# Kernel tuning notes

Hardware: AMD Instinct MI355X
Metric: run time of the kernel (lower is better)

Reference implementation:

```python
import jax, jax.numpy as jnp
import numpy as np

B, V, C = 2, 6, 96
D, H, W = 48, 48, 48
TH, TW = 96, 96
EPS = 1e-5


def _trilinear_sample_zeros(vol, gx, gy, gz):
    # vol: [B,C,D,H,W]; gx/gy/gz: normalized coords [D,H,W]; align_corners=False, zeros padding
    Dd, Hh, Ww = vol.shape[2], vol.shape[3], vol.shape[4]
    ix = ((gx + 1.0) * Ww - 1.0) * 0.5
    iy = ((gy + 1.0) * Hh - 1.0) * 0.5
    iz = ((gz + 1.0) * Dd - 1.0) * 0.5
    x0 = jnp.floor(ix); y0 = jnp.floor(iy); z0 = jnp.floor(iz)
    tx, ty, tz = ix - x0, iy - y0, iz - z0
    out = jnp.zeros(vol.shape, vol.dtype)
    for dz in (0, 1):
        for dy in (0, 1):
            for dx in (0, 1):
                xc, yc, zc = x0 + dx, y0 + dy, z0 + dz
                w = ((tx if dx else 1.0 - tx) * (ty if dy else 1.0 - ty)
                     * (tz if dz else 1.0 - tz))
                inb = ((xc >= 0) & (xc < Ww) & (yc >= 0) & (yc < Hh)
                       & (zc >= 0) & (zc < Dd))
                xi = jnp.clip(xc, 0, Ww - 1).astype(jnp.int32)
                yi = jnp.clip(yc, 0, Hh - 1).astype(jnp.int32)
                zi = jnp.clip(zc, 0, Dd - 1).astype(jnp.int32)
                val = vol[:, :, zi, yi, xi]  # [B,C,D,H,W]
                out = out + val * (w * inb)[None, None]
    return out


def _resize_bilinear(img, oh, ow):
    # torch F.interpolate(mode='bilinear', align_corners=False) semantics
    h, w = img.shape[-2], img.shape[-1]
    def idx(n_in, n_out):
        scale = n_in / n_out
        src = jnp.maximum(scale * (jnp.arange(n_out) + 0.5) - 0.5, 0.0)
        i0 = jnp.clip(jnp.floor(src).astype(jnp.int32), 0, n_in - 1)
        i1 = jnp.clip(i0 + 1, 0, n_in - 1)
        return i0, i1, (src - i0).astype(img.dtype)
    y0, y1, ty = idx(h, oh)
    x0, x1, tx = idx(w, ow)
    rows = img[..., y0, :] * (1.0 - ty)[:, None] + img[..., y1, :] * ty[:, None]
    return rows[..., x0] * (1.0 - tx) + rows[..., x1] * tx


def _project_one_view(vol, theta):
    # base grid per torch affine_grid(align_corners=False): pixel-center coords in [-1,1]
    zc = (jnp.arange(D) + 0.5) * (2.0 / D) - 1.0
    yc = (jnp.arange(H) + 0.5) * (2.0 / H) - 1.0
    xc = (jnp.arange(W) + 0.5) * (2.0 / W) - 1.0
    Z, Y, X = jnp.meshgrid(zc, yc, xc, indexing='ij')  # [D,H,W]
    c, s = jnp.cos(theta), jnp.sin(theta)
    gx = c * X + s * Z   # rotation about Y axis, rows [c,0,s],[0,1,0],[-s,0,c]
    gy = Y
    gz = -s * X + c * Z
    rotated = _trilinear_sample_zeros(vol, gx, gy, gz)  # [B,C,D,H,W]
    feat2d = rotated.mean(axis=2)                       # depth mean -> [B,C,H,W]
    return _resize_bilinear(feat2d, TH, TW)             # [B,C,TH,TW]


def _post(x, conv1_w, bn_gamma, bn_beta, conv2_w, conv2_b):
    dn = ('NCHW', 'OIHW', 'NCHW')
    x = jax.lax.conv_general_dilated(x, conv1_w, (1, 1), 'SAME', dimension_numbers=dn)
    mu = x.mean(axis=(0, 2, 3), keepdims=True)
    var = ((x - mu) ** 2).mean(axis=(0, 2, 3), keepdims=True)  # biased var, train-mode BN
    x = (x - mu) * jax.lax.rsqrt(var + EPS)
    x = x * bn_gamma[None, :, None, None] + bn_beta[None, :, None, None]
    x = jax.nn.gelu(x, approximate=False)
    x = jax.lax.conv_general_dilated(x, conv2_w, (1, 1), 'SAME', dimension_numbers=dn)
    return x + conv2_b[None, :, None, None]


def setup_inputs() -> dict:
    key = jax.random.key(0)
    k0, k1, k2 = jax.random.split(key, 3)
    voxel_tokens = jax.random.normal(k0, (B, D * H * W, C), jnp.float32)
    view_angles = jnp.linspace(0.0, 2.0 * np.pi, V + 1)[:-1].astype(jnp.float32)
    conv1_w = jax.random.normal(k1, (C, C, 3, 3), jnp.float32) / np.sqrt(C * 9.0)
    bn_gamma = jnp.ones((C,), jnp.float32)
    bn_beta = jnp.zeros((C,), jnp.float32)
    conv2_w = jax.random.normal(k2, (C, C, 1, 1), jnp.float32) / np.sqrt(C)
    conv2_b = jnp.zeros((C,), jnp.float32)
    return dict(voxel_tokens=voxel_tokens, view_angles=view_angles,
                conv1_w=conv1_w, bn_gamma=bn_gamma, bn_beta=bn_beta,
                conv2_w=conv2_w, conv2_b=conv2_b)


def reference(voxel_tokens, view_angles, conv1_w, bn_gamma, bn_beta, conv2_w, conv2_b):
    b = voxel_tokens.shape[0]
    vol = voxel_tokens.transpose(0, 2, 1).reshape(b, C, D, H, W)
    feats = jax.vmap(lambda th: _project_one_view(vol, th))(view_angles)  # [V,B,C,TH,TW]
    # BN stats are computed per-view (torch applies self.post inside the view loop)
    posted = jax.vmap(lambda f: _post(f, conv1_w, bn_gamma, bn_beta, conv2_w, conv2_b))(feats)
    return posted.transpose(1, 0, 2, 3, 4)  # [B,V,C,TH,TW]
```

## Files before the change

### kernel.cpp

```cpp
#include <hip/hip_runtime.h>
#include <math.h>

#define Bn 2
#define Vn 6
#define Cn 96
#define Dn 48
#define Hn 48
#define Wn 48
#define THn 96
#define TWn 96
#define EPSf 1e-5f

#define PD 98
#define NCI8 12

typedef __attribute__((ext_vector_type(8))) short s8v;
typedef __attribute__((ext_vector_type(4))) float f4v;

__device__ __forceinline__ unsigned short f2bf(float f) {
    unsigned int u = __builtin_bit_cast(unsigned int, f);
    u += 0x7FFFu + ((u >> 16) & 1u);
    return (unsigned short)(u >> 16);
}
__device__ __forceinline__ float bf2f(unsigned short h) {
    unsigned int u = ((unsigned int)h) << 16;
    return __builtin_bit_cast(float, u);
}
__device__ __forceinline__ void unpack8(uint4 r, float* f) {
    unsigned int w[4] = {r.x, r.y, r.z, r.w};
#pragma unroll
    for (int j = 0; j < 8; ++j)
        f[j] = bf2f((unsigned short)((w[j >> 1] >> ((j & 1) * 16)) & 0xFFFFu));
}
__device__ __forceinline__ uint4 pack8(const unsigned short* o) {
    uint4 pk;
    pk.x = (unsigned int)o[0] | ((unsigned int)o[1] << 16);
    pk.y = (unsigned int)o[2] | ((unsigned int)o[3] << 16);
    pk.z = (unsigned int)o[4] | ((unsigned int)o[5] << 16);
    pk.w = (unsigned int)o[6] | ((unsigned int)o[7] << 16);
    return pk;
}

__device__ __forceinline__ float gelu_f(float y) {
    float z = y * 0.70710678118654752f;
    float a = fabsf(z);
    float t = __builtin_amdgcn_rcpf(fmaf(0.3275911f, a, 1.0f));
    float e = __builtin_amdgcn_exp2f(-1.4426950408889634f * a * a);
    float p = t * fmaf(t, fmaf(t, fmaf(t, fmaf(t, 1.061405429f,
                                               -1.453152027f),
                                       1.421413741f),
                               -0.284496736f),
                       0.254829592f);
    float er = fmaf(-p, e, 1.0f);
    er = copysignf(er, z);
    return 0.5f * y * (1.0f + er);
}

__global__ __launch_bounds__(256) void k_pre(const float* __restrict__ tokens,
                                             unsigned short* __restrict__ tokB,
                                             const float* __restrict__ w1,
                                             const float* __restrict__ w2,
                                             unsigned short* __restrict__ wAtP,
                                             unsigned short* __restrict__ wCP,
                                             const float* __restrict__ angles,
                                             float4* __restrict__ wtabW,
                                             int4* __restrict__ wtabO) {
    if (blockIdx.x < 10368) {
        int idx = blockIdx.x * 256 + threadIdx.x;
        size_t base = (size_t)idx * 8;
        float4 f0 = *(const float4*)(tokens + base);
        float4 f1 = *(const float4*)(tokens + base + 4);
        unsigned short o[8] = {f2bf(f0.x), f2bf(f0.y), f2bf(f0.z), f2bf(f0.w),
                               f2bf(f1.x), f2bf(f1.y), f2bf(f1.z), f2bf(f1.w)};
        *(uint4*)(&tokB[base]) = pack8(o);
    } else if (blockIdx.x < 10728) {
        int i = (blockIdx.x - 10368) * 256 + threadIdx.x;
        if (i < 82944) {
            int e = i & 7;
            int u = i >> 3;
            int co = u % 96;
            int u2 = u / 96;
            int ci8 = u2 % NCI8;
            int tap = u2 / NCI8;
            wAtP[i] = f2bf(w1[(co * 96 + ci8 * 8 + e) * 9 + tap]);
        } else if (i < 92160) {
            int j = i - 82944;
            int e = j & 7;
            int u = j >> 3;
            int co = u % 96;
            int ci8 = u / 96;
            wCP[j] = f2bf(w2[co * 96 + ci8 * 8 + e]);
        }
    } else {
        int e = (blockIdx.x - 10728) * 256 + threadIdx.x;
        if (e >= 13824) return;
        int z = e % 48;
        int r = e / 48;
        int x = r % 48;
        int v = r / 48;

        float th = angles[v];
        float ct = cosf(th), st = sinf(th);
        float xr = (float)x + 0.5f - 24.0f;
        float zr = (float)z + 0.5f - 24.0f;
        float ix = ct * xr + st * zr + 23.5f;
        float iz = -st * xr + ct * zr + 23.5f;

        float x0f = floorf(ix), z0f = floorf(iz);
        float tx = ix - x0f, tz = iz - z0f;
        int x0 = (int)x0f, z0 = (int)z0f;
        float wx[2] = {1.0f - tx, tx};
        float wz[2] = {1.0f - tz, tz};

        float w[4];
        int o[4];
#pragma unroll
        for (int dz = 0; dz < 2; ++dz) {
            int zc = z0 + dz;
            bool zin = (zc >= 0) && (zc < Dn);
            int zi = min(max(zc, 0), Dn - 1);
#pragma unroll
            for (int dx = 0; dx < 2; ++dx) {
                int xc = x0 + dx;
                bool xin = (xc >= 0) && (xc < Wn);
                int xi = min(max(xc, 0), Wn - 1);
                int k = dz * 2 + dx;
                w[k] = wx[dx] * wz[dz] * ((zin && xin) ? 1.0f : 0.0f) * (1.0f / 48.0f);
                o[k] = (zi * 221184 + xi * 96) * 2;
            }
        }
        wtabW[e] = (float4){w[0], w[1], w[2], w[3]};
        wtabO[e] = (int4){o[0], o[1], o[2], o[3]};
    }
}

__global__ __launch_bounds__(256) void k_feat6(const unsigned short* __restrict__ tokB,
                                               const float4* __restrict__ wtabW,
                                               const int4* __restrict__ wtabO,
                                               unsigned short* __restrict__ featP) {
    int gid = blockIdx.x;
    int xcd = gid & 7;
    int pos = gid >> 3;
    int vblk = xcd * 648 + pos;
    int group = vblk / 9;
    int inner = vblk - group * 9;
    int v = group % 6;
    int by = group / 6;
    int y = by % 48;
    int b = by / 48;
    int vb = v * 2 + b;

    int t = threadIdx.x;
    int l = t & 63;
    int h = l >> 4;
    int s0 = inner * 64 + (t >> 6) * 16 + (l & 15);
    int c8 = s0 % NCI8;
    int x = s0 / NCI8;

    int tb0 = (v * 48 + x) * 48 + h * 12;
    const float4* tw = wtabW + tb0;
    const int4* to = wtabO + tb0;
    const char* tb = (const char*)tokB +
                     ((size_t)b * 10616832 + (size_t)y * 4608 + c8 * 8) * 2;

    float af[8] = {0.f, 0.f, 0.f, 0.f, 0.f, 0.f, 0.f, 0.f};
#pragma unroll 4
    for (int k = 0; k < 12; ++k) {
        float4 w = tw[k];
        int4 o = to[k];
        uint4 r0 = *(const uint4*)(tb + o.x);
        uint4 r1 = *(const uint4*)(tb + o.y);
        uint4 r2 = *(const uint4*)(tb + o.z);
        uint4 r3 = *(const uint4*)(tb + o.w);
        float f0[8], f1[8], f2[8], f3[8];
        unpack8(r0, f0); unpack8(r1, f1); unpack8(r2, f2); unpack8(r3, f3);
#pragma unroll
        for (int j = 0; j < 8; ++j) {
            af[j] += w.x * f0[j] + w.y * f1[j];
            af[j] += w.z * f2[j] + w.w * f3[j];
        }
    }
#pragma unroll
    for (int j = 0; j < 8; ++j) {
        af[j] += __shfl_xor(af[j], 16);
        af[j] += __shfl_xor(af[j], 32);
    }

    if (h == 0) {
        unsigned short o[8];
#pragma unroll
        for (int j = 0; j < 8; ++j) o[j] = f2bf(af[j]);
        size_t off = (((size_t)vb * Hn + y) * NCI8 + c8) * Wn + x;
        *(uint4*)(&featP[off * 8]) = pack8(o);
    }
}

__global__ __launch_bounds__(256) void k_resize(const unsigned short* __restrict__ featP,
                                                unsigned short* __restrict__ rz) {
    if (blockIdx.x >= 5184) {
        int hid = (blockIdx.x - 5184) * 256 + threadIdx.x;
        if (hid >= 55872) return;
        int p = hid % 388;
        int r2 = hid / 388;
        int c8 = r2 % NCI8;
        int vb = r2 / NCI8;
        int py, px;
        if (p < 98)      { py = 0;  px = p; }
        else if (p < 196){ py = 97; px = p - 98; }
        else { int q = p - 196; py = 1 + (q >> 1); px = (q & 1) ? 97 : 0; }
        size_t off = (((size_t)vb * PD + py) * NCI8 + c8) * PD + px;
        *(uint4*)(&rz[off * 8]) = (uint4){0u, 0u, 0u, 0u};
        return;
    }
    int idx = blockIdx.x * 256 + threadIdx.x;
    int x = idx % TWn;
    int r = idx / TWn;
    int c8i = r % NCI8; r /= NCI8;
    int y = r % THn;
    int vb = r / THn;

    float sy = fmaxf(0.5f * (y + 0.5f) - 0.5f, 0.0f);
    int y0 = min((int)sy, Hn - 1);
    int y1 = min(y0 + 1, Hn - 1);
    float ty = sy - (float)y0;
    float sx = fmaxf(0.5f * (x + 0.5f) - 0.5f, 0.0f);
    int x0 = min((int)sx, Wn - 1);
    int x1 = min(x0 + 1, Wn - 1);
    float tx = sx - (float)x0;

    const unsigned short* fb = featP + ((size_t)vb * Hn * NCI8 + c8i) * Wn * 8;
    const unsigned short* r0 = fb + (size_t)y0 * (NCI8 * Wn * 8);
    const unsigned short* r1 = fb + (size_t)y1 * (NCI8 * Wn * 8);
    uint4 q00 = *(const uint4*)(r0 + (size_t)x0 * 8);
    uint4 q01 = *(const uint4*)(r0 + (size_t)x1 * 8);
    uint4 q10 = *(const uint4*)(r1 + (size_t)x0 * 8);
    uint4 q11 = *(const uint4*)(r1 + (size_t)x1 * 8);
    float f00[8], f01[8], f10[8], f11[8];
    unpack8(q00, f00); unpack8(q01, f01); unpack8(q10, f10); unpack8(q11, f11);

    float w00 = (1.f - ty) * (1.f - tx), w01 = (1.f - ty) * tx;
    float w10 = ty * (1.f - tx),         w11 = ty * tx;

    unsigned short o[8];
#pragma unroll
    for (int j = 0; j < 8; ++j)
        o[j] = f2bf(w00 * f00[j] + w01 * f01[j] + w10 * f10[j] + w11 * f11[j]);

    size_t off = (((size_t)vb * PD + (y + 1)) * NCI8 + c8i) * PD + (x + 1);
    *(uint4*)(&rz[off * 8]) = pack8(o);
}

__global__ __launch_bounds__(256) void k_conv1(const unsigned short* __restrict__ rz,
                                               const unsigned short* __restrict__ wAtP,
                                               unsigned short* __restrict__ co1) {
    int blk = blockIdx.x;
    int n0 = blk * 64;
    int vb = n0 / 9216;
    int nl0 = n0 - vb * 9216;

    int t = threadIdx.x;
    int wv = t >> 6;
    int ch = wv & 1;
    int ns = wv >> 1;
    int l = t & 63;
    int l15 = l & 15, q = l >> 4;

    int nt0 = nl0 + ns * 32;
    int nl[2];
    const unsigned short* pB[2];
#pragma unroll
    for (int i = 0; i < 2; ++i) {
        nl[i] = nt0 + i * 16 + l15;
        int y = nl[i] / 96, x = nl[i] - y * 96;
        pB[i] = rz + ((((size_t)vb * PD + y) * NCI8) * PD + x) * 8;
    }

    f4v acc[2][3];
#pragma unroll
    for (int i = 0; i < 2; ++i)
#pragma unroll
        for (int mt = 0; mt < 3; ++mt) acc[i][mt] = (f4v){0.f, 0.f, 0.f, 0.f};

#pragma unroll
    for (int ks = 0; ks < 3; ++ks) {
        int ci8 = ks * 4 + q;
        const unsigned short* pb0 = pB[0] + (size_t)ci8 * (PD * 8);
        const unsigned short* pb1 = pB[1] + (size_t)ci8 * (PD * 8);
        const unsigned short* pa = wAtP + ((size_t)ci8 * 96 + ch * 48 + l15) * 8;
#pragma unroll
        for (int tap = 0; tap < 9; ++tap) {
            int dy = tap / 3, dx = tap % 3;
            size_t toff = ((size_t)dy * (NCI8 * PD) + dx) * 8;
            s8v b0 = *(const s8v*)(pb0 + toff);
            s8v b1 = *(const s8v*)(pb1 + toff);
            const unsigned short* ap = pa + (size_t)tap * (NCI8 * 96 * 8);
#pragma unroll
            for (int mt = 0; mt < 3; ++mt) {
                s8v a = *(const s8v*)(ap + (size_t)mt * (16 * 8));
                acc[0][mt] = __builtin_amdgcn_mfma_f32_16x16x32_bf16(a, b0, acc[0][mt], 0, 0, 0);
                acc[1][mt] = __builtin_amdgcn_mfma_f32_16x16x32_bf16(a, b1, acc[1][mt], 0, 0, 0);
            }
        }
    }

#pragma unroll
    for (int i = 0; i < 2; ++i) {
#pragma unroll
        for (int mt = 0; mt < 3; ++mt) {
            int co0 = ch * 48 + mt * 16 + q * 4;
            ushort4 pk;
            pk.x = f2bf(acc[i][mt][0]); pk.y = f2bf(acc[i][mt][1]);
            pk.z = f2bf(acc[i][mt][2]); pk.w = f2bf(acc[i][mt][3]);
            size_t off = (((size_t)vb * NCI8 + (co0 >> 3)) * 9216 + nl[i]) * 8 + (co0 & 7);
            *(ushort4*)(&co1[off]) = pk;
        }
    }
}

__global__ __launch_bounds__(256) void k_stats1(const unsigned short* __restrict__ co1,
                                                float* __restrict__ part) {
    int g = blockIdx.x >> 4;
    int chunk = blockIdx.x & 15;
    int v = g / NCI8;
    int c8 = g % NCI8;
    int t = threadIdx.x;

    float s[8] = {0,0,0,0,0,0,0,0}, ss[8] = {0,0,0,0,0,0,0,0};
    int m0 = chunk * 1152;
    for (int m = m0 + t; m < m0 + 1152; m += 256) {
        int bb = m / 9216;
        int n = m - bb * 9216;
        const unsigned short* p = co1 + (((size_t)(v * 2 + bb) * NCI8 + c8) * 9216 + n) * 8;
        uint4 raw = *(const uint4*)p;
        float f[8];
        unpack8(raw, f);
#pragma unroll
        for (int j = 0; j < 8; ++j) { s[j] += f[j]; ss[j] += f[j] * f[j]; }
    }
#pragma unroll
    for (int off = 1; off < 64; off <<= 1) {
#pragma unroll
        for (int j = 0; j < 8; ++j) {
            s[j]  += __shfl_xor(s[j],  off);
            ss[j] += __shfl_xor(ss[j], off);
        }
    }
    __shared__ float rs[4][8], rss[4][8];
    int wv = t >> 6;
    if ((t & 63) == 0) {
#pragma unroll
        for (int j = 0; j < 8; ++j) { rs[wv][j] = s[j]; rss[wv][j] = ss[j]; }
    }
    __syncthreads();
    if (t < 8) {
        int j = t;
        part[(size_t)blockIdx.x * 16 + j]     = rs[0][j] + rs[1][j] + rs[2][j] + rs[3][j];
        part[(size_t)blockIdx.x * 16 + 8 + j] = rss[0][j] + rss[1][j] + rss[2][j] + rss[3][j];
    }
}

__global__ __launch_bounds__(256) void k_conv2(const unsigned short* __restrict__ co1,
                                               const unsigned short* __restrict__ wCP,
                                               const float* __restrict__ part,
                                               const float* __restrict__ gamma,
                                               const float* __restrict__ beta,
                                               const float* __restrict__ b2,
                                               float* __restrict__ out) {
    __shared__ float ssc[96], ssh[96], sbias[96];

    int blk = blockIdx.x;
    int n0 = blk * 64;
    int vb = n0 / 9216;
    int nl0 = n0 - vb * 9216;
    int v = vb >> 1, b = vb & 1;

    int t = threadIdx.x;
    int wv = t >> 6;
    int l = t & 63;
    int l15 = l & 15, q = l >> 4;

    if (t < 96) {
        int c8 = t >> 3, j = t & 7;
        int g = v * NCI8 + c8;
        float S = 0.f, SS = 0.f;
#pragma unroll
        for (int c = 0; c < 16; ++c) {
            const float* pp = part + ((size_t)g * 16 + c) * 16;
            S += pp[j];
            SS += pp[8 + j];
        }
        const float invN = 1.0f / (float)(Bn * THn * TWn);
        float mu = S * invN;
        float var = SS * invN - mu * mu;
        float rstd = rsqrtf(fmaxf(var, 0.0f) + EPSf);
        float sc = rstd * gamma[t];
        ssc[t] = sc;
        ssh[t] = beta[t] - mu * sc;
        sbias[t] = b2[t];
    }
    __syncthreads();

    int n = nl0 + wv * 16 + l15;

    f4v acc[6];
#pragma unroll
    for (int mt = 0; mt < 6; ++mt) acc[mt] = (f4v){0.f, 0.f, 0.f, 0.f};

#pragma unroll
    for (int ks = 0; ks < 3; ++ks) {
        int ci8 = ks * 4 + q;
        int ci0 = ci8 * 8;
        float sc[8], sh[8];
#pragma unroll
        for (int j = 0; j < 8; ++j) { sc[j] = ssc[ci0 + j]; sh[j] = ssh[ci0 + j]; }

        const unsigned short* pb = co1 + (((size_t)vb * NCI8 + ci8) * 9216 + n) * 8;
        uint4 raw = *(const uint4*)pb;
        float f[8];
        unpack8(raw, f);
        unsigned short o[8];
#pragma unroll
        for (int j = 0; j < 8; ++j) {
            float yv = f[j] * sc[j] + sh[j];
            o[j] = f2bf(gelu_f(yv));
        }
        s8v bfr = __builtin_bit_cast(s8v, pack8(o));

        const unsigned short* pa = wCP + ((size_t)ci8 * 96 + l15) * 8;
#pragma unroll
        for (int mt = 0; mt < 6; ++mt) {
            s8v a = *(const s8v*)(pa + (size_t)mt * (16 * 8));
            acc[mt] = __builtin_amdgcn_mfma_f32_16x16x32_bf16(a, bfr, acc[mt], 0, 0, 0);
        }
    }

    size_t obase = ((size_t)(b * Vn + v) * Cn) * 9216;
#pragma unroll
    for (int mt = 0; mt < 6; ++mt) {
        int co0 = mt * 16 + q * 4;
#pragma unroll
        for (int reg = 0; reg < 4; ++reg) {
            int co = co0 + reg;
            out[obase + (size_t)co * 9216 + n] = acc[mt][reg] + sbias[co];
        }
    }
}

extern "C" void kernel_launch(void* const* d_in, const int* in_sizes, int n_in,
                              void* d_out, int out_size, void* d_ws, size_t ws_size,
                              hipStream_t stream) {
    const float* tokens = (const float*)d_in[0];
    const float* angles = (const float*)d_in[1];
    const float* w1     = (const float*)d_in[2];
    const float* gamma  = (const float*)d_in[3];
    const float* beta   = (const float*)d_in[4];
    const float* w2     = (const float*)d_in[5];
    const float* b2     = (const float*)d_in[6];
    float* out = (float*)d_out;

    char* ws = (char*)d_ws;
    unsigned short* featP = (unsigned short*)(ws);
    float* part           = (float*)(ws);
    unsigned short* tokB  = (unsigned short*)(ws + 5308416);
    unsigned short* rz    = (unsigned short*)(ws + 5308416);
    unsigned short* co1   = (unsigned short*)(ws + 27436032);
    float4* wtabW         = (float4*)(ws + 47775744);
    int4*  wtabO          = (int4*)(ws + 47996928);
    unsigned short* wAtP  = (unsigned short*)(ws + 48669696);
    unsigned short* wCP   = (unsigned short*)(ws + 48835584);

    k_pre<<<10782, 256, 0, stream>>>(tokens, tokB, w1, w2, wAtP, wCP,
                                     angles, wtabW, wtabO);
    k_feat6<<<5184, 256, 0, stream>>>(tokB, wtabW, wtabO, featP);
    k_resize<<<5403, 256, 0, stream>>>(featP, rz);
    k_conv1<<<1728, 256, 0, stream>>>(rz, wAtP, co1);
    k_stats1<<<1152, 256, 0, stream>>>(co1, part);
    k_conv2<<<1728, 256, 0, stream>>>(co1, wCP, part, gamma, beta, b2, out);
}
```

Measured before the change: 260.5 us.

## Use packed FP32 FMA in projection and stage conv2 output through LDS

The projection kernel now unpacks bf16 pairs straight into two-wide float vectors and accumulates with elementwise FMA, so the compiler can emit packed FP32 FMAs and simpler unpacking. The conv2 epilogue writes MFMA results into a padded shared-memory tile, then stores each channel row with float4 writes of 64 contiguous floats, instead of scattered 16-float segments per channel. The aim is to cut ALU work in the gather loop and make the large fp32 output write fully coalesced. The cost is about 25 KB of extra LDS per block and an added barrier. With the 65-float padding, the float4 LDS reads are not 16-byte aligned on odd rows, which may split into slower accesses.

```diff
diff --git a/kernel.cpp b/kernel.cpp
--- a/kernel.cpp
+++ b/kernel.cpp
@@ -16,6 +16,7 @@
 
 typedef __attribute__((ext_vector_type(8))) short s8v;
 typedef __attribute__((ext_vector_type(4))) float f4v;
+typedef __attribute__((ext_vector_type(2))) float f2v;
 
 __device__ __forceinline__ unsigned short f2bf(float f) {
     unsigned int u = __builtin_bit_cast(unsigned int, f);
@@ -31,6 +32,16 @@
 #pragma unroll
     for (int j = 0; j < 8; ++j)
         f[j] = bf2f((unsigned short)((w[j >> 1] >> ((j & 1) * 16)) & 0xFFFFu));
+}
+__device__ __forceinline__ void unpack8p(uint4 r, f2v* p) {
+    unsigned int w[4] = {r.x, r.y, r.z, r.w};
+#pragma unroll
+    for (int i = 0; i < 4; ++i) {
+        f2v t;
+        t.x = __builtin_bit_cast(float, w[i] << 16);
+        t.y = __builtin_bit_cast(float, w[i] & 0xFFFF0000u);
+        p[i] = t;
+    }
 }
 __device__ __forceinline__ uint4 pack8(const unsigned short* o) {
     uint4 pk;
@@ -134,7 +145,7 @@
     }
 }
 
-__global__ __launch_bounds__(256) void k_feat6(const unsigned short* __restrict__ tokB,
+__global__ __launch_bounds__(256) void k_feat7(const unsigned short* __restrict__ tokB,
                                                const float4* __restrict__ wtabW,
                                                const int4* __restrict__ wtabO,
                                                unsigned short* __restrict__ featP) {
@@ -163,7 +174,10 @@
     const char* tb = (const char*)tokB +
                      ((size_t)b * 10616832 + (size_t)y * 4608 + c8 * 8) * 2;
 
-    float af[8] = {0.f, 0.f, 0.f, 0.f, 0.f, 0.f, 0.f, 0.f};
+    f2v af[4];
+#pragma unroll
+    for (int i = 0; i < 4; ++i) af[i] = (f2v){0.f, 0.f};
+
 #pragma unroll 4
     for (int k = 0; k < 12; ++k) {
         float4 w = tw[k];
@@ -172,24 +186,30 @@
         uint4 r1 = *(const uint4*)(tb + o.y);
         uint4 r2 = *(const uint4*)(tb + o.z);
         uint4 r3 = *(const uint4*)(tb + o.w);
-        float f0[8], f1[8], f2[8], f3[8];
-        unpack8(r0, f0); unpack8(r1, f1); unpack8(r2, f2); unpack8(r3, f3);
-#pragma unroll
-        for (int j = 0; j < 8; ++j) {
-            af[j] += w.x * f0[j] + w.y * f1[j];
-            af[j] += w.z * f2[j] + w.w * f3[j];
-        }
-    }
-#pragma unroll
-    for (int j = 0; j < 8; ++j) {
-        af[j] += __shfl_xor(af[j], 16);
-        af[j] += __shfl_xor(af[j], 32);
+        f2v p0[4], p1[4], p2[4], p3[4];
+        unpack8p(r0, p0); unpack8p(r1, p1); unpack8p(r2, p2); unpack8p(r3, p3);
+        f2v wx = (f2v){w.x, w.x}, wy = (f2v){w.y, w.y};
+        f2v wz = (f2v){w.z, w.z}, ww = (f2v){w.w, w.w};
+#pragma unroll
+        for (int i = 0; i < 4; ++i) {
+            af[i] = __builtin_elementwise_fma(wx, p0[i], af[i]);
+            af[i] = __builtin_elementwise_fma(wy, p1[i], af[i]);
+            af[i] = __builtin_elementwise_fma(wz, p2[i], af[i]);
+            af[i] = __builtin_elementwise_fma(ww, p3[i], af[i]);
+        }
+    }
+#pragma unroll
+    for (int i = 0; i < 4; ++i) {
+        af[i].x += __shfl_xor(af[i].x, 16);
+        af[i].y += __shfl_xor(af[i].y, 16);
+        af[i].x += __shfl_xor(af[i].x, 32);
+        af[i].y += __shfl_xor(af[i].y, 32);
     }
 
     if (h == 0) {
         unsigned short o[8];
 #pragma unroll
-        for (int j = 0; j < 8; ++j) o[j] = f2bf(af[j]);
+        for (int j = 0; j < 8; ++j) o[j] = f2bf((j & 1) ? af[j >> 1].y : af[j >> 1].x);
         size_t off = (((size_t)vb * Hn + y) * NCI8 + c8) * Wn + x;
         *(uint4*)(&featP[off * 8]) = pack8(o);
     }
@@ -367,6 +387,7 @@
                                                const float* __restrict__ b2,
                                                float* __restrict__ out) {
     __shared__ float ssc[96], ssh[96], sbias[96];
+    __shared__ float sOut[96 * 65];
 
     int blk = blockIdx.x;
     int n0 = blk * 64;
@@ -434,15 +455,26 @@
         }
     }
 
-    size_t obase = ((size_t)(b * Vn + v) * Cn) * 9216;
+    int nloc = wv * 16 + l15;
 #pragma unroll
     for (int mt = 0; mt < 6; ++mt) {
         int co0 = mt * 16 + q * 4;
 #pragma unroll
         for (int reg = 0; reg < 4; ++reg) {
             int co = co0 + reg;
-            out[obase + (size_t)co * 9216 + n] = acc[mt][reg] + sbias[co];
-        }
+            sOut[co * 65 + nloc] = acc[mt][reg] + sbias[co];
+        }
+    }
+    __syncthreads();
+
+    size_t obase = ((size_t)(b * Vn + v) * Cn) * 9216 + nl0;
+#pragma unroll
+    for (int r = 0; r < 6; ++r) {
+        int cid = r * 256 + t;
+        int row = cid >> 4;
+        int chunk = cid & 15;
+        float4 vv = *(const float4*)(&sOut[row * 65 + chunk * 4]);
+        *(float4*)(&out[obase + (size_t)row * 9216 + chunk * 4]) = vv;
     }
 }
 
@@ -471,7 +503,7 @@
 
     k_pre<<<10782, 256, 0, stream>>>(tokens, tokB, w1, w2, wAtP, wCP,
                                      angles, wtabW, wtabO);
-    k_feat6<<<5184, 256, 0, stream>>>(tokB, wtabW, wtabO, featP);
+    k_feat7<<<5184, 256, 0, stream>>>(tokB, wtabW, wtabO, featP);
     k_resize<<<5403, 256, 0, stream>>>(featP, rz);
     k_conv1<<<1728, 256, 0, stream>>>(rz, wAtP, co1);
     k_stats1<<<1152, 256, 0, stream>>>(co1, part);
```

Result: no change. 261.0 us (+0.2%).
